# Kernel optimization log

Measured on AMD Instinct MI355X. Metric: run time of the kernel, lower is better.

Reference implementation:

```python
import jax, jax.numpy as jnp
import numpy as np

B, D = 512, 512
NOBJ, NWRD = 12, 16  # word_feat rows act as 'objects', object_feat rows as 'words' (arg swap in SentiGAT.forward)
N_OW = NOBJ + NWRD
EPS = 1e-12


def _with_self_loops(src, dst, n):
    return (np.concatenate([src, np.arange(n)]), np.concatenate([dst, np.arange(n)]))

_src = np.tile(np.arange(NOBJ), NWRD)                 # arange(n_obj).repeat(n_words) in torch == tile
_dst = np.repeat(np.arange(NWRD), NOBJ) + NOBJ        # repeat_interleave + offset
SRC_OW, DST_OW = map(jnp.asarray, _with_self_loops(_src, _dst, N_OW))

_E5 = np.array([[0,0,0,0,1,1,1,1,2,2,2,2,3,3,3,3,4,4,4,4],
                [1,2,3,4,0,2,3,4,0,1,3,4,0,1,2,4,0,1,2,3]])
SRC5, DST5 = map(jnp.asarray, _with_self_loops(_E5[0], _E5[1], 5))


def gat_conv(x, src, dst, W, a_src, a_dst, bias, concat, num_nodes):
    """PyG GATConv (add_self_loops already in src/dst, negative_slope=0.2, dropout=0)."""
    heads, out_dim = a_src.shape
    h = (x @ W).reshape(num_nodes, heads, out_dim)
    e = jax.nn.leaky_relu((h * a_src).sum(-1)[src] + (h * a_dst).sum(-1)[dst], 0.2)  # [E, heads]
    m = jax.ops.segment_max(e, dst, num_segments=num_nodes)
    p = jnp.exp(e - m[dst])
    alpha = p / jax.ops.segment_sum(p, dst, num_segments=num_nodes)[dst]             # softmax over incoming edges
    out = jax.ops.segment_sum(alpha[:, :, None] * h[src], dst, num_segments=num_nodes)
    out = out.reshape(num_nodes, heads * out_dim) if concat else out.mean(axis=1)
    return out + bias


def _ind_norm(f):
    # add_feature_indicator + F.normalize(p=2, dim=1, eps=1e-12)
    v = (f.sum(axis=1) != 0).astype(f.dtype)[:, None]
    g = jnp.concatenate([f, v], axis=1)
    return g / jnp.maximum(jnp.linalg.norm(g, axis=1, keepdims=True), EPS)


def setup_inputs() -> dict:
    k = jax.random.split(jax.random.key(0), 32)
    r = lambda i, s: jax.random.normal(k[i], s, dtype=jnp.float32)
    sc = 0.05
    return {
        "text_feat": r(0, (B, D)), "image_feat": r(1, (B, D)), "imgtxt_feat": r(2, (B, D)),
        "face_feat": r(3, (B, D)), "word_feat": r(4, (B, NOBJ, D)), "object_feat": r(5, (B, NWRD, D)),
        "ow_W": r(6, (D, 2 * D)) * sc, "ow_asrc": r(7, (2, D)) * sc, "ow_adst": r(8, (2, D)) * sc,
        "ow_b": jnp.zeros((D,), jnp.float32),
        "g1_W": r(9, (D + 1, D)) * sc, "g1_asrc": r(10, (1, D)) * sc, "g1_adst": r(11, (1, D)) * sc,
        "g1_b": jnp.zeros((D,), jnp.float32),
        "g2_W": r(12, (D, D)) * sc, "g2_asrc": r(13, (1, D)) * sc, "g2_adst": r(14, (1, D)) * sc,
        "g2_b": jnp.zeros((D,), jnp.float32),
        "m1_W": r(15, (5 * D, D)) * sc, "m1_b": jnp.zeros((D,), jnp.float32),
        "m2_W": r(16, (D, 3)) * sc, "m2_b": jnp.zeros((3,), jnp.float32),
    }


def reference(text_feat, image_feat, imgtxt_feat, face_feat, word_feat, object_feat,
              ow_W, ow_asrc, ow_adst, ow_b,
              g1_W, g1_asrc, g1_adst, g1_b,
              g2_W, g2_asrc, g2_adst, g2_b,
              m1_W, m1_b, m2_W, m2_b):
    # --- ObjectWordGAT (object_embs=word_feat, word_embs=object_feat per SentiGAT.forward) ---
    def per_sample(obj, wrd):
        x = jnp.concatenate([obj, wrd], axis=0)                       # [N_OW, D]
        h = gat_conv(x, SRC_OW, DST_OW, ow_W, ow_asrc, ow_adst, ow_b, False, N_OW)
        uo, uw = h[:NOBJ], h[NOBJ:]
        attn = jax.nn.softmax(uo @ uw.T, axis=1)                      # [NOBJ, NWRD]
        return (attn @ uw).mean(axis=0)                               # [D]
    aligned = jax.vmap(per_sample)(word_feat, object_feat)            # [B, D]

    feats = [_ind_norm(f) for f in (text_feat, image_feat, imgtxt_feat, face_feat, aligned)]
    x = jnp.stack(feats, axis=1)                                      # [B, 5, D+1]

    # edge_attr (cosine sims) is ignored by GATConv when edge_dim is None
    def graph5(xb):
        h = gat_conv(xb, SRC5, DST5, g1_W, g1_asrc, g1_adst, g1_b, True, 5)
        h = jax.nn.relu(h)
        return gat_conv(h, SRC5, DST5, g2_W, g2_asrc, g2_adst, g2_b, True, 5)
    x = jax.vmap(graph5)(x)                                           # [B, 5, D]

    fused = x.reshape(B, 5 * D)
    hid = jax.nn.relu(fused @ m1_W + m1_b)                            # dropout = identity (eval)
    return hid @ m2_W + m2_b                                          # [B, 3] logits
```

## Files before the change

kernel.cpp:

```cpp
#include <hip/hip_runtime.h>
#include <hip/hip_bf16.h>
#include <math.h>


#define B_SAMP 512

typedef short short8 __attribute__((ext_vector_type(8)));
typedef float floatx4 __attribute__((ext_vector_type(4)));

__device__ __forceinline__ float lrelu02(float x) { return x > 0.f ? x : 0.2f * x; }

__device__ __forceinline__ unsigned short cvt_bf16(float f) {
    union { float f; unsigned int u; } v; v.f = f;
    unsigned int u = v.u;
    return (unsigned short)((u + 0x7FFFu + ((u >> 16) & 1u)) >> 16);
}

__global__ __launch_bounds__(256) void prep(
    const float* __restrict__ ow_W, const float* __restrict__ ow_asrc,
    const float* __restrict__ ow_adst,
    const float* __restrict__ g1_W, const float* __restrict__ g2_W,
    const float* __restrict__ m1_W,
    float* __restrict__ vg, unsigned short* __restrict__ owWt,
    unsigned short* __restrict__ g1Wt, unsigned short* __restrict__ g2Wt,
    unsigned short* __restrict__ m1Wt)
{
    __shared__ float T[32][33];
    const int tid = threadIdx.x;
    int bid = blockIdx.x;

    if (bid < 128) {
        const int lane = tid & 63;
        const int gw = bid * 4 + (tid >> 6);
        for (int idx = gw; idx < 2048; idx += 512) {
            int t = idx >> 9, k = idx & 511;
            const float* a = (t < 2) ? (ow_asrc + t * 512) : (ow_adst + (t - 2) * 512);
            const float* wr = ow_W + (size_t)k * 1024 + (t & 1) * 512;
            float s = 0.f;
#pragma unroll
            for (int j = 0; j < 8; ++j) s += wr[lane + 64 * j] * a[lane + 64 * j];
            for (int off = 32; off > 0; off >>= 1) s += __shfl_down(s, off, 64);
            if (lane == 0) vg[idx] = s;
        }
        return;
    }
    bid -= 128;
    const float* W; int ldw, K, Kpad, koff, ktiles; float scale; unsigned short* Wt;
    if (bid < 256)        { W = ow_W;       ldw = 1024; K = 512;  Kpad = 1024; koff = 0;   scale = 0.5f; Wt = owWt; ktiles = 16; }
    else if (bid < 512)   { bid -= 256;  W = ow_W + 512; ldw = 1024; K = 512;  Kpad = 1024; koff = 512; scale = 0.5f; Wt = owWt; ktiles = 16; }
    else if (bid < 784)   { bid -= 512;  W = g1_W; ldw = 512; K = 513;  Kpad = 544;  koff = 0; scale = 1.f; Wt = g1Wt; ktiles = 17; }
    else if (bid < 1040)  { bid -= 784;  W = g2_W; ldw = 512; K = 512;  Kpad = 512;  koff = 0; scale = 1.f; Wt = g2Wt; ktiles = 16; }
    else                  { bid -= 1040; W = m1_W; ldw = 512; K = 2560; Kpad = 2560; koff = 0; scale = 1.f; Wt = m1Wt; ktiles = 80; }
    const int k0 = (bid % ktiles) * 32;
    const int n0 = (bid / ktiles) * 32;
    {
        int kr = tid >> 3, nc = (tid & 7) * 4;
        float4 v = make_float4(0.f, 0.f, 0.f, 0.f);
        if (k0 + kr < K) v = *(const float4*)(W + (size_t)(k0 + kr) * ldw + n0 + nc);
        T[nc + 0][kr] = v.x * scale; T[nc + 1][kr] = v.y * scale;
        T[nc + 2][kr] = v.z * scale; T[nc + 3][kr] = v.w * scale;
    }
    __syncthreads();
    {
        int nr = tid >> 3, kc = (tid & 7) * 4;
        ushort4 w;
        w.x = cvt_bf16(T[nr][kc + 0]);
        w.y = cvt_bf16(T[nr][kc + 1]);
        w.z = cvt_bf16(T[nr][kc + 2]);
        w.w = cvt_bf16(T[nr][kc + 3]);
        *(ushort4*)(Wt + (size_t)(n0 + nr) * Kpad + koff + k0 + kc) = w;
    }
}

__global__ __launch_bounds__(256) void fusedA(
    const float* __restrict__ wf, const float* __restrict__ of,
    const float* __restrict__ vg, const unsigned short* __restrict__ Bt,
    const float* __restrict__ ow_b,
    const float* __restrict__ tf, const float* __restrict__ im,
    const float* __restrict__ it, const float* __restrict__ fa,
    unsigned short* __restrict__ x5)
{
    __shared__ __align__(16) char smem[156608];
    float* Xs = (float*)smem;
    unsigned short* Z = (unsigned short*)(smem + 57792);
    char* BsB = smem + 123840;
    float* sml = (float*)BsB;

    const int b = blockIdx.x;
    const int tid = threadIdx.x;
    const int lane = tid & 63;
    const int wid = tid >> 6;

    for (int idx = tid; idx < 28 * 128; idx += 256) {
        int n = idx >> 7, c = (idx & 127) * 4;
        const float* src = (n < 12) ? (wf + ((size_t)b * 12 + n) * 512)
                                    : (of + ((size_t)b * 16 + (n - 12)) * 512);
        *(float4*)&Xs[n * 516 + c] = *(const float4*)(src + c);
    }
    __syncthreads();

    float* ss = sml;
    float* sd = sml + 56;
    float* alpha = sml + 112;
    for (int p = wid; p < 112; p += 4) {
        int n = p >> 2, t = p & 3;
        const float* vv = vg + t * 512;
        float s = 0.f;
#pragma unroll
        for (int j = 0; j < 8; ++j) s += Xs[n * 516 + lane + 64 * j] * vv[lane + 64 * j];
        for (int off = 32; off > 0; off >>= 1) s += __shfl_down(s, off, 64);
        if (lane == 0) { if (t < 2) ss[n * 2 + t] = s; else sd[n * 2 + t - 2] = s; }
    }
    __syncthreads();
    if (tid < 32) {
        int w = tid >> 1, h = tid & 1;
        float sdv = sd[(12 + w) * 2 + h];
        float e[13], mx = -1e30f;
        for (int j = 0; j < 12; ++j) { e[j] = lrelu02(ss[j * 2 + h] + sdv); mx = fmaxf(mx, e[j]); }
        e[12] = lrelu02(ss[(12 + w) * 2 + h] + sdv); mx = fmaxf(mx, e[12]);
        float den = 0.f;
        for (int j = 0; j < 13; ++j) { e[j] = expf(e[j] - mx); den += e[j]; }
        float inv = 1.f / den;
        for (int j = 0; j < 13; ++j) alpha[(w * 2 + h) * 13 + j] = e[j] * inv;
    }
    __syncthreads();

    short8 rb[8];
#pragma unroll
    for (int i = 0; i < 8; ++i) {
        int idx = tid + i * 256;
        int row = idx >> 2, seg = idx & 3;
        rb[i] = *(const short8*)(Bt + (size_t)row * 1024 + seg * 8);
    }

    for (int idx = tid; idx < 12 * 1024; idx += 256) {
        int n = idx >> 10, dd = idx & 1023;
        Z[n * 1032 + dd] = cvt_bf16(Xs[n * 516 + (dd & 511)]);
    }
    for (int c = tid; c < 1024; c += 256) {
        int h = c >> 9, d = c & 511;
        float xr[12];
#pragma unroll
        for (int j = 0; j < 12; ++j) xr[j] = Xs[j * 516 + d];
#pragma unroll 4
        for (int w = 0; w < 16; ++w) {
            const float* alp = &alpha[(w * 2 + h) * 13];
            float a = alp[12] * Xs[(12 + w) * 516 + d];
#pragma unroll
            for (int j = 0; j < 12; ++j) a += alp[j] * xr[j];
            Z[(12 + w) * 1032 + c] = cvt_bf16(a);
        }
    }
    for (int idx = tid; idx < 4 * 1024; idx += 256)
        Z[(28 + (idx >> 10)) * 1032 + (idx & 1023)] = 0;
    __syncthreads();

    const int wn = wid * 128;
    const int fr = lane & 15;
    const int slot = lane >> 4;
    floatx4 acc[2][8];
#pragma unroll
    for (int i = 0; i < 2; ++i)
#pragma unroll
        for (int j = 0; j < 8; ++j) acc[i][j] = (floatx4){0.f, 0.f, 0.f, 0.f};

    for (int k0 = 0; k0 < 1024; k0 += 32) {
#pragma unroll
        for (int i = 0; i < 8; ++i) {
            int idx = tid + i * 256;
            int row = idx >> 2, seg = idx & 3;
            int sw = seg ^ ((row >> 2) & 3);
            *(short8*)(BsB + row * 64 + sw * 16) = rb[i];
        }
        __syncthreads();
        if (k0 + 32 < 1024) {
#pragma unroll
            for (int i = 0; i < 8; ++i) {
                int idx = tid + i * 256;
                int row = idx >> 2, seg = idx & 3;
                rb[i] = *(const short8*)(Bt + (size_t)row * 1024 + (k0 + 32) + seg * 8);
            }
        }
        short8 af[2];
#pragma unroll
        for (int i = 0; i < 2; ++i)
            af[i] = *(const short8*)&Z[(i * 16 + fr) * 1032 + k0 + slot * 8];
#pragma unroll
        for (int j = 0; j < 8; ++j) {
            int row = wn + j * 16 + fr;
            int sw = slot ^ ((row >> 2) & 3);
            short8 bw = *(const short8*)(BsB + row * 64 + sw * 16);
#pragma unroll
            for (int i = 0; i < 2; ++i)
                acc[i][j] = __builtin_amdgcn_mfma_f32_16x16x32_bf16(af[i], bw, acc[i][j], 0, 0, 0);
        }
        __syncthreads();
    }

    const int fq = lane >> 4;
#pragma unroll
    for (int i = 0; i < 2; ++i) {
#pragma unroll
        for (int j = 0; j < 8; ++j) {
#pragma unroll
            for (int q = 0; q < 4; ++q) {
                int row = i * 16 + fq * 4 + q;
                int col = wn + j * 16 + fr;
                if (row < 28) Xs[row * 516 + col] = acc[i][j][q] + ow_b[col];
            }
        }
    }
    __syncthreads();

    float* S = sml;
    float* w16 = sml + 192;
    float* al = sml + 208;
    if (tid < 192) {
        int i = tid >> 4, j = tid & 15;
        float s = 0.f;
        for (int d = 0; d < 128; ++d) {
            float4 a = *(const float4*)&Xs[i * 516 + d * 4];
            float4 c = *(const float4*)&Xs[(12 + j) * 516 + d * 4];
            s += a.x * c.x + a.y * c.y + a.z * c.z + a.w * c.w;
        }
        S[i * 16 + j] = s;
    }
    __syncthreads();
    if (tid < 12) {
        float mx = -1e30f;
        for (int j = 0; j < 16; ++j) mx = fmaxf(mx, S[tid * 16 + j]);
        float den = 0.f;
        for (int j = 0; j < 16; ++j) { float p = expf(S[tid * 16 + j] - mx); S[tid * 16 + j] = p; den += p; }
        float inv = 1.f / den;
        for (int j = 0; j < 16; ++j) S[tid * 16 + j] *= inv;
    }
    __syncthreads();
    if (tid < 16) {
        float s = 0.f;
        for (int i = 0; i < 12; ++i) s += S[i * 16 + tid];
        w16[tid] = s * (1.f / 12.f);
    }
    __syncthreads();
    for (int d = tid; d < 512; d += 256) {
        float s = 0.f;
#pragma unroll
        for (int j = 0; j < 16; ++j) s += w16[j] * Xs[(12 + j) * 516 + d];
        al[d] = s;
    }
    __syncthreads();

    for (int f = wid; f < 5; f += 4) {
        const float* src = (f == 0) ? tf : (f == 1) ? im : (f == 2) ? it : (f == 3) ? fa : nullptr;
        float vals[8];
        float sum = 0.f, sq = 0.f;
#pragma unroll
        for (int j = 0; j < 8; ++j) {
            float v = (f < 4) ? src[(size_t)b * 512 + lane + 64 * j] : al[lane + 64 * j];
            vals[j] = v;
            sum += v;
            sq += v * v;
        }
#pragma unroll
        for (int off = 32; off > 0; off >>= 1) {
            sum += __shfl_xor(sum, off, 64);
            sq  += __shfl_xor(sq,  off, 64);
        }
        float v = (sum != 0.f) ? 1.f : 0.f;
        float nrm = fmaxf(sqrtf(sq + v * v), 1e-12f);
        float inv = 1.f / nrm;
        unsigned short* dst = x5 + ((size_t)b * 5 + f) * 544;
#pragma unroll
        for (int j = 0; j < 8; ++j) dst[lane + 64 * j] = cvt_bf16(vals[j] * inv);
        if (lane == 0) dst[512] = cvt_bf16(v * inv);
        else if (lane < 32) dst[512 + lane] = 0;
    }
}

template <int BM, int BN, int RELU, int SPLITK>
__global__ __launch_bounds__(256) void gemm_v2(
    const unsigned short* __restrict__ A, int lda,
    const unsigned short* __restrict__ Bt, int ldbt,
    float* __restrict__ C, int ldc,
    int M, int N, int K,
    const float* __restrict__ bias)
{
    constexpr int WM = BM / 2, WN = BN / 2;
    constexpr int MF = WM / 16, NF = WN / 16;
    constexpr int CA = BM / 64, CB = BN / 64;

    __shared__ unsigned short As[2][BM][40];
    __shared__ unsigned short Bs[2][BN][40];

    const int tid = threadIdx.x;
    const int m0 = blockIdx.x * BM;
    const int n0 = blockIdx.y * BN;
    const int lane = tid & 63;
    const int wid = tid >> 6;
    const int wm = (wid & 1) * WM;
    const int wn = (wid >> 1) * WN;
    const int fr = lane & 15;
    const int kq = (lane >> 4) * 8;

    const int srow = tid >> 2;
    const int scol = (tid & 3) * 8;

    const int kchunk = K / SPLITK;
    const int kbeg = (SPLITK > 1) ? blockIdx.z * kchunk : 0;
    const int kend = kbeg + kchunk;
    if (SPLITK > 1) C += (size_t)blockIdx.z * M * ldc;

    short8 ra[CA], rb[CB];
#define LOADAB(K0)                                                                   \
    do {                                                                             \
        _Pragma("unroll")                                                            \
        for (int c = 0; c < CA; ++c)                                                 \
            ra[c] = *(const short8*)(A + (size_t)(m0 + srow + c * 64) * lda + (K0) + scol); \
        _Pragma("unroll")                                                            \
        for (int c = 0; c < CB; ++c)                                                 \
            rb[c] = *(const short8*)(Bt + (size_t)(n0 + srow + c * 64) * ldbt + (K0) + scol); \
    } while (0)

    LOADAB(kbeg);

    floatx4 acc[MF][NF];
#pragma unroll
    for (int i = 0; i < MF; ++i)
#pragma unroll
        for (int j = 0; j < NF; ++j) acc[i][j] = (floatx4){0.f, 0.f, 0.f, 0.f};

    int t = 0;
    for (int k0 = kbeg; k0 < kend; k0 += 32, t ^= 1) {
#pragma unroll
        for (int c = 0; c < CA; ++c) *(short8*)&As[t][srow + c * 64][scol] = ra[c];
#pragma unroll
        for (int c = 0; c < CB; ++c) *(short8*)&Bs[t][srow + c * 64][scol] = rb[c];
        __syncthreads();
        if (k0 + 32 < kend) LOADAB(k0 + 32);

        short8 af[MF], bw[NF];
#pragma unroll
        for (int i = 0; i < MF; ++i)
            af[i] = *(const short8*)&As[t][wm + i * 16 + fr][kq];
#pragma unroll
        for (int j = 0; j < NF; ++j)
            bw[j] = *(const short8*)&Bs[t][wn + j * 16 + fr][kq];
#pragma unroll
        for (int i = 0; i < MF; ++i)
#pragma unroll
            for (int j = 0; j < NF; ++j)
                acc[i][j] = __builtin_amdgcn_mfma_f32_16x16x32_bf16(
                    af[i], bw[j], acc[i][j], 0, 0, 0);
    }
#undef LOADAB

    const int fq = lane >> 4;
#pragma unroll
    for (int i = 0; i < MF; ++i) {
#pragma unroll
        for (int j = 0; j < NF; ++j) {
#pragma unroll
            for (int q = 0; q < 4; ++q) {
                int row = m0 + wm + i * 16 + fq * 4 + q;
                int col = n0 + wn + j * 16 + fr;
                float v = acc[i][j][q];
                if (SPLITK == 1 && bias) v += bias[col];
                if (RELU) v = fmaxf(v, 0.f);
                C[(size_t)row * ldc + col] = v;
            }
        }
    }
}

template <int RELU>
__global__ __launch_bounds__(256) void g5_gat(
    const float* __restrict__ Hg,
    const float* __restrict__ asrc, const float* __restrict__ adst,
    const float* __restrict__ bias, unsigned short* __restrict__ outp)
{
    const int b = blockIdx.x;
    __shared__ float ss[5], sd[5];
    __shared__ float alpha[5][5];

    const int tid = threadIdx.x;
    const int lane = tid & 63;
    const int wave = tid >> 6;
    const float* Hb = Hg + (size_t)b * 5 * 512;

    for (int p = wave; p < 10; p += 4) {
        int n = p >> 1, ty = p & 1;
        const float* hv = Hb + n * 512;
        const float* av = ty ? adst : asrc;
        float s = 0.f;
#pragma unroll
        for (int j = 0; j < 8; ++j) s += hv[lane + 64 * j] * av[lane + 64 * j];
        for (int off = 32; off > 0; off >>= 1) s += __shfl_down(s, off, 64);
        if (lane == 0) { if (ty) sd[n] = s; else ss[n] = s; }
    }
    __syncthreads();

    if (tid < 5) {
        int dn = tid;
        float e[5];
        float mx = -1e30f;
        for (int s = 0; s < 5; ++s) {
            e[s] = lrelu02(ss[s] + sd[dn]);
            mx = fmaxf(mx, e[s]);
        }
        float den = 0.f;
        for (int s = 0; s < 5; ++s) { e[s] = expf(e[s] - mx); den += e[s]; }
        float inv = 1.f / den;
        for (int s = 0; s < 5; ++s) alpha[dn][s] = e[s] * inv;
    }
    __syncthreads();

    for (int d = tid; d < 512; d += 256) {
        float h0 = Hb[0 * 512 + d], h1 = Hb[1 * 512 + d], h2 = Hb[2 * 512 + d];
        float h3 = Hb[3 * 512 + d], h4 = Hb[4 * 512 + d];
        float bd = bias[d];
#pragma unroll
        for (int dn = 0; dn < 5; ++dn) {
            float v = alpha[dn][0] * h0 + alpha[dn][1] * h1 + alpha[dn][2] * h2 +
                      alpha[dn][3] * h3 + alpha[dn][4] * h4 + bd;
            if (RELU) v = fmaxf(v, 0.f);
            outp[((size_t)b * 5 + dn) * 512 + d] = cvt_bf16(v);
        }
    }
}

__global__ __launch_bounds__(64) void final2(
    const float* __restrict__ parts, const float* __restrict__ b1,
    const float* __restrict__ w, const float* __restrict__ bvec,
    float* __restrict__ out)
{
    const int b = blockIdx.x;
    const int lane = threadIdx.x;
    float a0 = 0.f, a1 = 0.f, a2 = 0.f;
#pragma unroll
    for (int j = 0; j < 8; ++j) {
        int d = lane + 64 * j;
        size_t o = (size_t)b * 512 + d;
        float x = parts[o] + parts[262144 + o] + parts[524288 + o] + parts[786432 + o] + b1[d];
        x = fmaxf(x, 0.f);
        a0 += x * w[d * 3 + 0];
        a1 += x * w[d * 3 + 1];
        a2 += x * w[d * 3 + 2];
    }
    for (int off = 32; off > 0; off >>= 1) {
        a0 += __shfl_down(a0, off, 64);
        a1 += __shfl_down(a1, off, 64);
        a2 += __shfl_down(a2, off, 64);
    }
    if (lane == 0) {
        out[b * 3 + 0] = a0 + bvec[0];
        out[b * 3 + 1] = a1 + bvec[1];
        out[b * 3 + 2] = a2 + bvec[2];
    }
}

extern "C" void kernel_launch(void* const* d_in, const int* in_sizes, int n_in,
                              void* d_out, int out_size, void* d_ws, size_t ws_size,
                              hipStream_t stream) {
    const float* text   = (const float*)d_in[0];
    const float* image  = (const float*)d_in[1];
    const float* imgtxt = (const float*)d_in[2];
    const float* face   = (const float*)d_in[3];
    const float* word   = (const float*)d_in[4];
    const float* obj    = (const float*)d_in[5];
    const float* ow_W    = (const float*)d_in[6];
    const float* ow_asrc = (const float*)d_in[7];
    const float* ow_adst = (const float*)d_in[8];
    const float* ow_b    = (const float*)d_in[9];
    const float* g1_W    = (const float*)d_in[10];
    const float* g1_asrc = (const float*)d_in[11];
    const float* g1_adst = (const float*)d_in[12];
    const float* g1_b    = (const float*)d_in[13];
    const float* g2_W    = (const float*)d_in[14];
    const float* g2_asrc = (const float*)d_in[15];
    const float* g2_adst = (const float*)d_in[16];
    const float* g2_b    = (const float*)d_in[17];
    const float* m1_W    = (const float*)d_in[18];
    const float* m1_b    = (const float*)d_in[19];
    const float* m2_W    = (const float*)d_in[20];
    const float* m2_b    = (const float*)d_in[21];

    float* ws = (float*)d_ws;
    float* vg = ws;
    unsigned short* owWt = (unsigned short*)(ws + 2048);
    unsigned short* g1Wt = owWt + 524288;
    unsigned short* g2Wt = g1Wt + 278528;
    unsigned short* m1Wt = g2Wt + 262144;
    unsigned short* x5b  = m1Wt + 1310720;
    unsigned short* h1b  = x5b + 1392640;
    unsigned short* fsb  = h1b + 1310720;
    float* hg   = (float*)(fsb + 1310720);
    float* hidp = hg + 1310720;

    prep<<<2448, 256, 0, stream>>>(ow_W, ow_asrc, ow_adst, g1_W, g2_W, m1_W,
                                   vg, owWt, g1Wt, g2Wt, m1Wt);

    fusedA<<<B_SAMP, 256, 0, stream>>>(word, obj, vg, owWt, ow_b,
                                       text, image, imgtxt, face, x5b);

    gemm_v2<64, 64, 0, 1><<<dim3(40, 8), 256, 0, stream>>>(
        x5b, 544, g1Wt, 544, hg, 512, 2560, 512, 544, nullptr);
    g5_gat<1><<<B_SAMP, 256, 0, stream>>>(hg, g1_asrc, g1_adst, g1_b, h1b);
    gemm_v2<64, 64, 0, 1><<<dim3(40, 8), 256, 0, stream>>>(
        h1b, 512, g2Wt, 512, hg, 512, 2560, 512, 512, nullptr);
    g5_gat<0><<<B_SAMP, 256, 0, stream>>>(hg, g2_asrc, g2_adst, g2_b, fsb);

    gemm_v2<64, 64, 0, 4><<<dim3(8, 8, 4), 256, 0, stream>>>(
        fsb, 2560, m1Wt, 2560, hidp, 512, 512, 512, 2560, nullptr);
    final2<<<B_SAMP, 64, 0, stream>>>(hidp, m1_b, m2_W, m2_b, (float*)d_out);
}
```

Measured before the change: 150.8 us.

## Quadruple fusedA block size to 1024 threads and redistribute per-sample work

Launches the per-sample fused kernel with 1024 threads instead of 256. Each wave now owns a 32-column slice of the 1024-wide MFMA projection instead of 128, so every phase gets four times as many waves per block. The object-word similarity dot products move from one-thread-per-pair serial loops to wave-wide shuffle reductions, and the bf16 conversion and zeroing stores are packed in pairs. The aim is more latency hiding and parallelism within the single resident block per CU. In exchange there are more block-wide barriers with many waves, and the launch-bounds change may constrain registers.

```diff
diff --git a/kernel.cpp b/kernel.cpp
--- a/kernel.cpp
+++ b/kernel.cpp
@@ -72,7 +72,7 @@
     }
 }
 
-__global__ __launch_bounds__(256) void fusedA(
+__global__ __launch_bounds__(1024, 4) void fusedA(
     const float* __restrict__ wf, const float* __restrict__ of,
     const float* __restrict__ vg, const unsigned short* __restrict__ Bt,
     const float* __restrict__ ow_b,
@@ -91,7 +91,7 @@
     const int lane = tid & 63;
     const int wid = tid >> 6;
 
-    for (int idx = tid; idx < 28 * 128; idx += 256) {
+    for (int idx = tid; idx < 28 * 128; idx += 1024) {
         int n = idx >> 7, c = (idx & 127) * 4;
         const float* src = (n < 12) ? (wf + ((size_t)b * 12 + n) * 512)
                                     : (of + ((size_t)b * 16 + (n - 12)) * 512);
@@ -102,7 +102,7 @@
     float* ss = sml;
     float* sd = sml + 56;
     float* alpha = sml + 112;
-    for (int p = wid; p < 112; p += 4) {
+    for (int p = wid; p < 112; p += 16) {
         int n = p >> 2, t = p & 3;
         const float* vv = vg + t * 512;
         float s = 0.f;
@@ -125,19 +125,24 @@
     }
     __syncthreads();
 
-    short8 rb[8];
-#pragma unroll
-    for (int i = 0; i < 8; ++i) {
-        int idx = tid + i * 256;
+    short8 rb[2];
+#pragma unroll
+    for (int i = 0; i < 2; ++i) {
+        int idx = tid + i * 1024;
         int row = idx >> 2, seg = idx & 3;
         rb[i] = *(const short8*)(Bt + (size_t)row * 1024 + seg * 8);
     }
 
-    for (int idx = tid; idx < 12 * 1024; idx += 256) {
-        int n = idx >> 10, dd = idx & 1023;
-        Z[n * 1032 + dd] = cvt_bf16(Xs[n * 516 + (dd & 511)]);
-    }
-    for (int c = tid; c < 1024; c += 256) {
+    for (int idx = tid; idx < 12 * 512; idx += 1024) {
+        int n = idx >> 9, p = idx & 511;
+        int d = (p * 2) & 511;
+        ushort2 v;
+        v.x = cvt_bf16(Xs[n * 516 + d]);
+        v.y = cvt_bf16(Xs[n * 516 + d + 1]);
+        *(ushort2*)&Z[n * 1032 + p * 2] = v;
+    }
+    {
+        int c = tid;
         int h = c >> 9, d = c & 511;
         float xr[12];
 #pragma unroll
@@ -151,23 +156,23 @@
             Z[(12 + w) * 1032 + c] = cvt_bf16(a);
         }
     }
-    for (int idx = tid; idx < 4 * 1024; idx += 256)
-        Z[(28 + (idx >> 10)) * 1032 + (idx & 1023)] = 0;
-    __syncthreads();
-
-    const int wn = wid * 128;
+    for (int idx = tid; idx < 4 * 512; idx += 1024)
+        *(ushort2*)&Z[(28 + (idx >> 9)) * 1032 + (idx & 511) * 2] = make_ushort2(0, 0);
+    __syncthreads();
+
+    const int wn = wid * 32;
     const int fr = lane & 15;
     const int slot = lane >> 4;
-    floatx4 acc[2][8];
+    floatx4 acc[2][2];
 #pragma unroll
     for (int i = 0; i < 2; ++i)
 #pragma unroll
-        for (int j = 0; j < 8; ++j) acc[i][j] = (floatx4){0.f, 0.f, 0.f, 0.f};
+        for (int j = 0; j < 2; ++j) acc[i][j] = (floatx4){0.f, 0.f, 0.f, 0.f};
 
     for (int k0 = 0; k0 < 1024; k0 += 32) {
 #pragma unroll
-        for (int i = 0; i < 8; ++i) {
-            int idx = tid + i * 256;
+        for (int i = 0; i < 2; ++i) {
+            int idx = tid + i * 1024;
             int row = idx >> 2, seg = idx & 3;
             int sw = seg ^ ((row >> 2) & 3);
             *(short8*)(BsB + row * 64 + sw * 16) = rb[i];
@@ -175,25 +180,27 @@
         __syncthreads();
         if (k0 + 32 < 1024) {
 #pragma unroll
-            for (int i = 0; i < 8; ++i) {
-                int idx = tid + i * 256;
+            for (int i = 0; i < 2; ++i) {
+                int idx = tid + i * 1024;
                 int row = idx >> 2, seg = idx & 3;
                 rb[i] = *(const short8*)(Bt + (size_t)row * 1024 + (k0 + 32) + seg * 8);
             }
         }
-        short8 af[2];
+        short8 af[2], bw[2];
 #pragma unroll
         for (int i = 0; i < 2; ++i)
             af[i] = *(const short8*)&Z[(i * 16 + fr) * 1032 + k0 + slot * 8];
 #pragma unroll
-        for (int j = 0; j < 8; ++j) {
+        for (int j = 0; j < 2; ++j) {
             int row = wn + j * 16 + fr;
             int sw = slot ^ ((row >> 2) & 3);
-            short8 bw = *(const short8*)(BsB + row * 64 + sw * 16);
-#pragma unroll
-            for (int i = 0; i < 2; ++i)
-                acc[i][j] = __builtin_amdgcn_mfma_f32_16x16x32_bf16(af[i], bw, acc[i][j], 0, 0, 0);
-        }
+            bw[j] = *(const short8*)(BsB + row * 64 + sw * 16);
+        }
+#pragma unroll
+        for (int i = 0; i < 2; ++i)
+#pragma unroll
+            for (int j = 0; j < 2; ++j)
+                acc[i][j] = __builtin_amdgcn_mfma_f32_16x16x32_bf16(af[i], bw[j], acc[i][j], 0, 0, 0);
         __syncthreads();
     }
 
@@ -201,7 +208,7 @@
 #pragma unroll
     for (int i = 0; i < 2; ++i) {
 #pragma unroll
-        for (int j = 0; j < 8; ++j) {
+        for (int j = 0; j < 2; ++j) {
 #pragma unroll
             for (int q = 0; q < 4; ++q) {
                 int row = i * 16 + fq * 4 + q;
@@ -215,15 +222,15 @@
     float* S = sml;
     float* w16 = sml + 192;
     float* al = sml + 208;
-    if (tid < 192) {
-        int i = tid >> 4, j = tid & 15;
+    for (int p = wid; p < 192; p += 16) {
+        int i = p >> 4, j = p & 15;
+        const float* ua = &Xs[i * 516 + lane * 8];
+        const float* uc = &Xs[(12 + j) * 516 + lane * 8];
         float s = 0.f;
-        for (int d = 0; d < 128; ++d) {
-            float4 a = *(const float4*)&Xs[i * 516 + d * 4];
-            float4 c = *(const float4*)&Xs[(12 + j) * 516 + d * 4];
-            s += a.x * c.x + a.y * c.y + a.z * c.z + a.w * c.w;
-        }
-        S[i * 16 + j] = s;
+#pragma unroll
+        for (int d = 0; d < 8; ++d) s += ua[d] * uc[d];
+        for (int off = 32; off > 0; off >>= 1) s += __shfl_down(s, off, 64);
+        if (lane == 0) S[i * 16 + j] = s;
     }
     __syncthreads();
     if (tid < 12) {
@@ -241,7 +248,8 @@
         w16[tid] = s * (1.f / 12.f);
     }
     __syncthreads();
-    for (int d = tid; d < 512; d += 256) {
+    if (tid < 512) {
+        int d = tid;
         float s = 0.f;
 #pragma unroll
         for (int j = 0; j < 16; ++j) s += w16[j] * Xs[(12 + j) * 516 + d];
@@ -249,7 +257,7 @@
     }
     __syncthreads();
 
-    for (int f = wid; f < 5; f += 4) {
+    for (int f = wid; f < 5; f += 16) {
         const float* src = (f == 0) ? tf : (f == 1) ? im : (f == 2) ? it : (f == 3) ? fa : nullptr;
         float vals[8];
         float sum = 0.f, sq = 0.f;
@@ -498,8 +506,8 @@
     prep<<<2448, 256, 0, stream>>>(ow_W, ow_asrc, ow_adst, g1_W, g2_W, m1_W,
                                    vg, owWt, g1Wt, g2Wt, m1Wt);
 
-    fusedA<<<B_SAMP, 256, 0, stream>>>(word, obj, vg, owWt, ow_b,
-                                       text, image, imgtxt, face, x5b);
+    fusedA<<<B_SAMP, 1024, 0, stream>>>(word, obj, vg, owWt, ow_b,
+                                        text, image, imgtxt, face, x5b);
 
     gemm_v2<64, 64, 0, 1><<<dim3(40, 8), 256, 0, stream>>>(
         x5b, 544, g1Wt, 544, hg, 512, 2560, 512, 544, nullptr);
```

Result: faster. 132.0 us (-12.4%).
